# Optimization experiments

Hardware: AMD Instinct MI355X
Metric: run time of the kernel (lower is better)

The kernel has to match this reference:

```python
import jax, jax.numpy as jnp
import numpy as np
import math

N_HEAD = 16
MEM_LEN = 512


def setup_inputs() -> dict:
    key = jax.random.key(0)
    ks = jax.random.split(key, 4)
    B, T, C = 4, 2048, 1024
    x = jax.random.normal(ks[0], (B, T, C), dtype=jnp.float32)
    W_attn = jax.random.normal(ks[1], (C, 3 * C), dtype=jnp.float32) * (1.0 / math.sqrt(C))
    b_attn = jnp.zeros((3 * C,), dtype=jnp.float32)
    W_proj = jax.random.normal(ks[2], (C, C), dtype=jnp.float32) * (1.0 / math.sqrt(C))
    b_proj = jnp.zeros((C,), dtype=jnp.float32)
    return {"x": x, "W_attn": W_attn, "b_attn": b_attn, "W_proj": W_proj, "b_proj": b_proj}


def reference(x, W_attn, b_attn, W_proj, b_proj):
    B, T, C = x.shape
    H = N_HEAD
    Dh = C // H
    # fused qkv projection (torch Linear with weight stored as [in, out])
    qkv = x @ W_attn + b_attn                      # [B, T, 3C]
    q, k, v = jnp.split(qkv, 3, axis=-1)
    q = q.reshape(B, T, H, Dh).transpose(0, 2, 1, 3)  # [B, H, T, Dh]
    k = k.reshape(B, T, H, Dh).transpose(0, 2, 1, 3)
    v = v.reshape(B, T, H, Dh).transpose(0, 2, 1, 3)
    # manual attention: QK^T, causal mask, softmax, att @ V
    att = jnp.einsum('bhtd,bhsd->bhts', q, k) * (1.0 / math.sqrt(Dh))  # [B,H,T,T]
    causal = jnp.tril(jnp.ones((T, T), dtype=bool))
    att = jnp.where(causal[None, None, :, :], att, jnp.finfo(att.dtype).min)
    att = jax.nn.softmax(att, axis=-1)
    y = jnp.einsum('bhts,bhsd->bhtd', att, v)      # [B, H, T, Dh]
    y = y.transpose(0, 2, 1, 3).reshape(B, T, C)
    out = y @ W_proj + b_proj                      # resid_dropout is identity (p=0 / eval)
    new_memory = x[:, -MEM_LEN:, :]
    return out, new_memory
```

## Files before the change

### kernel.cpp

```cpp
#include <hip/hip_runtime.h>
#include <hip/hip_bf16.h>

typedef __bf16 bf16;
typedef __bf16 bf16x8 __attribute__((ext_vector_type(8)));
typedef __bf16 bf16x4v __attribute__((ext_vector_type(4)));
typedef float f32x4 __attribute__((ext_vector_type(4)));
typedef float f32x16 __attribute__((ext_vector_type(16)));
typedef float float4v __attribute__((ext_vector_type(4)));
typedef unsigned int uint32x4 __attribute__((ext_vector_type(4)));

#define MFMA16(a, b, c) __builtin_amdgcn_mfma_f32_16x16x32_bf16(a, b, c, 0, 0, 0)
#define MFMA32(a, b, c) __builtin_amdgcn_mfma_f32_32x32x16_bf16(a, b, c, 0, 0, 0)

#define SCALE_Q 0.1803368801111f

__device__ __forceinline__ void async_load16(const bf16* g, bf16* l) {
    __builtin_amdgcn_global_load_lds(
        (const __attribute__((address_space(1))) void*)g,
        (__attribute__((address_space(3))) void*)l,
        16, 0, 0);
}

__device__ __forceinline__ unsigned int pack2bf(float a, float b) {
    bf16 x = (bf16)a, y = (bf16)b;
    unsigned short ux = __builtin_bit_cast(unsigned short, x);
    unsigned short uy = __builtin_bit_cast(unsigned short, y);
    return (unsigned int)ux | ((unsigned int)uy << 16);
}

__global__ void k_pre(const float* __restrict__ x, const float* __restrict__ W_attn,
                      const float* __restrict__ W_proj,
                      bf16* __restrict__ xb, float* __restrict__ out_mem,
                      bf16* __restrict__ WaT, bf16* __restrict__ WpT) {
    __shared__ float tile[32][33];
    int bid = blockIdx.x;
    if (bid < 8192) {
        int i = bid * 256 + threadIdx.x;
        float4v v = ((const float4v*)x)[i];
        bf16x4v o;
        o.x = (bf16)v.x; o.y = (bf16)v.y; o.z = (bf16)v.z; o.w = (bf16)v.w;
        ((bf16x4v*)xb)[i] = o;
        int rem = i & 524287;
        if (rem >= 393216) {
            int b = i >> 19;
            ((float4v*)out_mem)[(size_t)b * 131072 + (rem - 393216)] = v;
        }
        return;
    }
    const float* W;  bf16* WT;  int R, Cc, bx, by;
    if (bid < 8192 + 3072) {
        int idx = bid - 8192;
        W = W_attn; WT = WaT; R = 1024; Cc = 3072; bx = idx % 96; by = idx / 96;
    } else {
        int idx = bid - 11264;
        W = W_proj; WT = WpT; R = 1024; Cc = 1024; bx = idx & 31; by = idx >> 5;
    }
    int r0 = by * 32, c0 = bx * 32;
    int tx = threadIdx.x & 31, ty = threadIdx.x >> 5;
#pragma unroll
    for (int i = 0; i < 32; i += 8)
        tile[ty + i][tx] = W[(size_t)(r0 + ty + i) * Cc + c0 + tx];
    __syncthreads();
#pragma unroll
    for (int i = 0; i < 32; i += 8)
        WT[(size_t)(c0 + ty + i) * R + r0 + tx] = (bf16)tile[tx][ty + i];
}

#define STAGE64(db, k0) { \
    async_load16(Asrc + (k0),          &As[db][tid8]);         \
    async_load16(Asrc + 32768 + (k0),  &As[db][2048 + tid8]);  \
    async_load16(Asrc + 65536 + (k0),  &As[db][4096 + tid8]);  \
    async_load16(Asrc + 98304 + (k0),  &As[db][6144 + tid8]);  \
    async_load16(Bsrc + (k0),          &Bs[db][tid8]);         \
    async_load16(Bsrc + 32768 + (k0),  &Bs[db][2048 + tid8]);  \
    async_load16(Bsrc + 65536 + (k0),  &Bs[db][4096 + tid8]);  \
    async_load16(Bsrc + 98304 + (k0),  &Bs[db][6144 + tid8]);  }

#define GEMM_BODY64                                                                      \
    STAGE64(0, 0)                                                                        \
    STAGE64(1, 64)                                                                       \
    asm volatile("s_waitcnt vmcnt(8)" ::: "memory");                                     \
    __builtin_amdgcn_sched_barrier(0);                                                   \
    __builtin_amdgcn_s_barrier();                                                        \
    __builtin_amdgcn_sched_barrier(0);                                                   \
    for (int t = 0; t < 16; ++t) {                                                       \
        int db = t & 1;                                                                  \
        _Pragma("unroll")                                                                \
        for (int kc = 0; kc < 2; ++kc) {                                                 \
            bf16x8 af[4], bfr[4];                                                        \
            _Pragma("unroll")                                                            \
            for (int mi = 0; mi < 4; ++mi)                                               \
                af[mi] = *(const bf16x8*)&As[db][(wr * 64 + mi * 16 + lrow) * 64 +       \
                                                 ((kc * 4 + lks) ^ (lrow & 7)) * 8];     \
            _Pragma("unroll")                                                            \
            for (int ni = 0; ni < 4; ++ni)                                               \
                bfr[ni] = *(const bf16x8*)&Bs[db][(wc * 64 + ni * 16 + lrow) * 64 +      \
                                                  ((kc * 4 + lks) ^ (lrow & 7)) * 8];    \
            __builtin_amdgcn_s_setprio(1);                                               \
            _Pragma("unroll")                                                            \
            for (int mi = 0; mi < 4; ++mi)                                               \
                _Pragma("unroll")                                                        \
                for (int ni = 0; ni < 4; ++ni)                                           \
                    acc[mi][ni] = MFMA16(af[mi], bfr[ni], acc[mi][ni]);                  \
            __builtin_amdgcn_s_setprio(0);                                               \
        }                                                                                \
        asm volatile("s_waitcnt lgkmcnt(0)" ::: "memory");                               \
        __builtin_amdgcn_sched_barrier(0);                                               \
        __builtin_amdgcn_s_barrier();                 \
        __builtin_amdgcn_sched_barrier(0);                                               \
        if (t + 2 < 16) {                                                                \
            STAGE64(db, (t + 2) * 64)                \
            asm volatile("s_waitcnt vmcnt(8)" ::: "memory");        \
        } else {                                                                         \
            asm volatile("s_waitcnt vmcnt(0)" ::: "memory");                             \
        }                                                                                \
        __builtin_amdgcn_sched_barrier(0);                                               \
        __builtin_amdgcn_s_barrier();                        \
        __builtin_amdgcn_sched_barrier(0);                                               \
    }

__global__ __launch_bounds__(256, 2) void k_gemm_qkv(
    const bf16* __restrict__ A, const bf16* __restrict__ BT,
    const float* __restrict__ bias,
    bf16* __restrict__ qo, bf16* __restrict__ ko, bf16* __restrict__ vo) {
    __shared__ __align__(16) bf16 As[2][8192];
    __shared__ __align__(16) bf16 Bs[2][8192];
    int orig = blockIdx.y * 24 + blockIdx.x;
    int wg = (orig & 7) * 192 + (orig >> 3);
    int row0 = (wg / 24) * 128;
    int col0 = (wg % 24) * 128;
    int tid = threadIdx.x;
    int lane = tid & 63, w = tid >> 6;
    int wr = w >> 1, wc = w & 1;
    int lrow = lane & 15, lks = lane >> 4;
    int tid8 = tid * 8;
    f32x4 acc[4][4] = {};
    const bf16* Asrc = A + (size_t)(row0 + (tid >> 3)) * 1024 + ((tid & 7) ^ ((tid >> 3) & 7)) * 8;
    const bf16* Bsrc = BT + (size_t)(col0 + (tid >> 3)) * 1024 + ((tid & 7) ^ ((tid >> 3) & 7)) * 8;

    GEMM_BODY64

    int trow = row0 + wr * 64 + lks * 4;
    int tcol = col0 + wc * 64 + lrow;
#pragma unroll
    for (int m = 0; m < 4; ++m)
#pragma unroll
        for (int n = 0; n < 4; ++n) {
            int cg = tcol + n * 16;
            float bi = bias[cg];
#pragma unroll
            for (int j = 0; j < 4; ++j) {
                int rg = trow + m * 16 + j;
                float val = acc[m][n][j] + bi;
                int b = rg >> 11, tt = rg & 2047;
                if (cg < 1024) {
                    int h = cg >> 6, d = cg & 63;
                    size_t base = (size_t)(b * 16 + h) * 131072;
                    size_t idx = base + (size_t)((((tt >> 5) * 4 + (d >> 4)) * 64 + ((d >> 3) & 1) * 32 + (tt & 31)) * 8 + (d & 7));
                    qo[idx] = (bf16)(val * SCALE_Q);
                } else if (cg < 2048) {
                    int c2 = cg - 1024;
                    int h = c2 >> 6, d = c2 & 63;
                    size_t base = (size_t)(b * 16 + h) * 131072;
                    size_t idx = base + (size_t)((((tt >> 5) * 4 + (d >> 4)) * 64 + ((d >> 3) & 1) * 32 + (tt & 31)) * 8 + (d & 7));
                    ko[idx] = (bf16)val;
                } else {
                    int c2 = cg - 2048;
                    int h = c2 >> 6, d = c2 & 63;
                    size_t base = (size_t)(b * 16 + h) * 131072;
                    size_t idx = base + (size_t)(((((tt >> 6) * 4 + ((tt >> 4) & 3)) * 2 + (d >> 5)) * 64 + ((tt >> 3) & 1) * 32 + (d & 31)) * 8 + (tt & 7));
                    vo[idx] = (bf16)val;
                }
            }
        }
}

__global__ __launch_bounds__(256, 2) void k_gemm_proj(
    const bf16* __restrict__ A, const bf16* __restrict__ BT,
    const float* __restrict__ bias, float* __restrict__ out) {
    __shared__ __align__(16) bf16 As[2][8192];
    __shared__ __align__(16) bf16 Bs[2][8192];
    int orig = blockIdx.y * 8 + blockIdx.x;
    int wg = (orig & 7) * 64 + (orig >> 3);
    int row0 = (wg >> 3) * 128;
    int col0 = (wg & 7) * 128;
    int tid = threadIdx.x;
    int lane = tid & 63, w = tid >> 6;
    int wr = w >> 1, wc = w & 1;
    int lrow = lane & 15, lks = lane >> 4;
    int tid8 = tid * 8;
    f32x4 acc[4][4] = {};
    const bf16* Asrc = A + (size_t)(row0 + (tid >> 3)) * 1024 + ((tid & 7) ^ ((tid >> 3) & 7)) * 8;
    const bf16* Bsrc = BT + (size_t)(col0 + (tid >> 3)) * 1024 + ((tid & 7) ^ ((tid >> 3) & 7)) * 8;

    GEMM_BODY64

    int trow = row0 + wr * 64 + lks * 4;
    int tcol = col0 + wc * 64 + lrow;
#pragma unroll
    for (int m = 0; m < 4; ++m)
#pragma unroll
        for (int n = 0; n < 4; ++n) {
            int cg = tcol + n * 16;
            float bi = bias[cg];
#pragma unroll
            for (int j = 0; j < 4; ++j) {
                int rg = trow + m * 16 + j;
                out[(size_t)rg * 1024 + cg] = acc[m][n][j] + bi;
            }
        }
}

__global__ __launch_bounds__(256, 2) void k_attn(
    const bf16* __restrict__ qp, const bf16* __restrict__ kp,
    const bf16* __restrict__ vp, bf16* __restrict__ y) {
    __shared__ __align__(16) bf16 Ks[2][4096];
    __shared__ __align__(16) bf16 Vs[2][4096];
    int id = blockIdx.x;
    int bxp = (id >> 3) & 7;
    int bh = (id & 7) + 8 * (id >> 6);
    int b = bh >> 4;
    int lane = threadIdx.x & 63, w = threadIdx.x >> 6;
    int tl = lane & 31, hi = lane >> 5;
    int lane8 = lane * 8;
    const bf16* Qb = qp + (size_t)bh * 131072;
    const bf16* Kb = kp + (size_t)bh * 131072;
    const bf16* Vb = vp + (size_t)bh * 131072;

    for (int qpass = 0; qpass < 2; ++qpass) {
        int qt0 = (qpass ? 15 - bxp : bxp) * 128;
        int trow0 = qt0 + w * 32;
        int t_g = trow0 + tl;

        bf16x8 qf[4];
        int qs = (trow0 >> 5) * 4;
#pragma unroll
        for (int kc = 0; kc < 4; ++kc)
            qf[kc] = *(const bf16x8*)&Qb[(qs + kc) * 512 + lane8];

        f32x16 o[2] = {};
        float m = -1e30f, l = 0.f;
        int ntb = (qt0 >> 6) + 2;
        int cur = 0;

#pragma unroll
        for (int i = 0; i < 2; ++i) {
            int u = 2 * w + i;
            async_load16(Kb + (size_t)u * 512 + lane8, &Ks[0][u * 512]);
            async_load16(Vb + (size_t)u * 512 + lane8, &Vs[0][u * 512]);
        }
        __syncthreads();

        for (int ti = 0; ti < ntb; ++ti) {
            int s0 = ti * 64;
            if (ti + 1 < ntb) {
#pragma unroll
                for (int i = 0; i < 2; ++i) {
                    int u = 2 * w + i;
                    async_load16(Kb + (size_t)((ti + 1) * 8 + u) * 512 + lane8, &Ks[cur ^ 1][u * 512]);
                    async_load16(Vb + (size_t)((ti + 1) * 8 + u) * 512 + lane8, &Vs[cur ^ 1][u * 512]);
                }
            }
            if (s0 < trow0 + 32) {
                f32x16 accs[2] = {};
                __builtin_amdgcn_s_setprio(1);
#pragma unroll
                for (int st = 0; st < 2; ++st)
#pragma unroll
                    for (int kc = 0; kc < 4; ++kc) {
                        bf16x8 kf = *(const bf16x8*)&Ks[cur][(st * 4 + kc) * 512 + lane8];
                        accs[st] = MFMA32(kf, qf[kc], accs[st]);
                    }
                __builtin_amdgcn_s_setprio(0);

                if (s0 + 63 > trow0) {
#pragma unroll
                    for (int st = 0; st < 2; ++st)
#pragma unroll
                        for (int r = 0; r < 16; ++r) {
                            int s = s0 + st * 32 + (r & 3) + 8 * (r >> 2) + 4 * hi;
                            if (s > t_g) accs[st][r] = -1e30f;
                        }
                }
                float pmax = -1e30f;
#pragma unroll
                for (int st = 0; st < 2; ++st)
#pragma unroll
                    for (int r = 0; r < 16; ++r)
                        pmax = fmaxf(pmax, accs[st][r]);
                pmax = fmaxf(pmax, __shfl_xor(pmax, 32));
                if (!__all(pmax <= m + 8.0f)) {
                    float mn = fmaxf(m, pmax);
                    float corr = __builtin_amdgcn_exp2f(m - mn);
                    m = mn;
                    l *= corr;
#pragma unroll
                    for (int dt = 0; dt < 2; ++dt)
#pragma unroll
                        for (int r = 0; r < 16; ++r)
                            o[dt][r] *= corr;
                }
                float ls = 0.f;
#pragma unroll
                for (int st = 0; st < 2; ++st)
#pragma unroll
                    for (int r = 0; r < 16; ++r) {
                        float p = __builtin_amdgcn_exp2f(accs[st][r] - m);
                        accs[st][r] = p;
                        ls += p;
                    }
                ls += __shfl_xor(ls, 32);
                l += ls;

                unsigned int pk[16];
#pragma unroll
                for (int st = 0; st < 2; ++st)
#pragma unroll
                    for (int q = 0; q < 8; ++q)
                        pk[st * 8 + q] = pack2bf(accs[st][2 * q], accs[st][2 * q + 1]);
                unsigned int rv[8];
#pragma unroll
                for (int st = 0; st < 2; ++st)
#pragma unroll
                    for (int i = 0; i < 4; ++i) {
                        int base = st * 8 + (i < 2 ? i : i + 2);
                        unsigned int send = hi ? pk[base] : pk[base + 2];
                        rv[st * 4 + i] = __shfl_xor(send, 32);
                    }
                __builtin_amdgcn_s_setprio(1);
#pragma unroll
                for (int c = 0; c < 4; ++c) {
                    const int st = c >> 1, c2 = c & 1;
                    uint32x4 pw;
                    pw.x = hi ? rv[st * 4 + 2 * c2]     : pk[st * 8 + 4 * c2];
                    pw.y = hi ? rv[st * 4 + 2 * c2 + 1] : pk[st * 8 + 4 * c2 + 1];
                    pw.z = hi ? pk[st * 8 + 4 * c2 + 2] : rv[st * 4 + 2 * c2];
                    pw.w = hi ? pk[st * 8 + 4 * c2 + 3] : rv[st * 4 + 2 * c2 + 1];
                    bf16x8 pf = __builtin_bit_cast(bf16x8, pw);
#pragma unroll
                    for (int dt = 0; dt < 2; ++dt) {
                        bf16x8 vf = *(const bf16x8*)&Vs[cur][(c * 2 + dt) * 512 + lane8];
                        o[dt] = MFMA32(vf, pf, o[dt]);
                    }
                }
                __builtin_amdgcn_s_setprio(0);
            }
            __syncthreads();
            cur ^= 1;
        }

        int hcol = (bh & 15) * 64;
        float inv = 1.0f / l;
        bf16* yr = y + (size_t)(b * 2048 + t_g) * 1024 + hcol;
#pragma unroll
        for (int dt = 0; dt < 2; ++dt)
#pragma unroll
            for (int rq = 0; rq < 4; ++rq) {
                bf16x4v ov;
#pragma unroll
                for (int ri = 0; ri < 4; ++ri)
                    ov[ri] = (bf16)(o[dt][rq * 4 + ri] * inv);
                *(bf16x4v*)&yr[dt * 32 + rq * 8 + hi * 4] = ov;
            }
    }
}

extern "C" void kernel_launch(void* const* d_in, const int* in_sizes, int n_in,
                              void* d_out, int out_size, void* d_ws, size_t ws_size,
                              hipStream_t stream) {
    const float* x = (const float*)d_in[0];
    const float* W_attn = (const float*)d_in[1];
    const float* b_attn = (const float*)d_in[2];
    const float* W_proj = (const float*)d_in[3];
    const float* b_proj = (const float*)d_in[4];
    float* out = (float*)d_out;
    float* out_mem = out + (size_t)8388608;

    char* ws = (char*)d_ws;
    bf16* xb  = (bf16*)(ws);
    bf16* WaT = (bf16*)(ws + ((size_t)16 << 20));
    bf16* WpT = (bf16*)(ws + ((size_t)22 << 20));
    bf16* q   = (bf16*)(ws + ((size_t)24 << 20));
    bf16* k   = (bf16*)(ws + ((size_t)40 << 20));
    bf16* vT  = (bf16*)(ws + ((size_t)56 << 20));
    bf16* y   = (bf16*)(ws + ((size_t)72 << 20));

    k_pre<<<12288, 256, 0, stream>>>(x, W_attn, W_proj, xb, out_mem, WaT, WpT);
    k_gemm_qkv<<<dim3(24, 64), 256, 0, stream>>>(xb, WaT, b_attn, q, k, vT);
    k_attn<<<512, 256, 0, stream>>>(q, k, vT, y);
    k_gemm_proj<<<dim3(8, 64), 256, 0, stream>>>(y, WpT, b_proj, out);
}
```

Before: 184.1 us.

## Pre-pack GEMM operands in MFMA fragment order and load directly into registers

The preprocessing kernel and the attention epilogue now write x, both weight matrices and the attention output in a packed layout where each 16-row, 32-k fragment is contiguous in per-lane order. The two GEMMs then drop LDS staging and barriers and load fragments straight from global memory into registers, double-buffered in registers. This removes LDS traffic and synchronization, but it gives up LDS-based reuse across waves, so each wave reads its A and B fragments from global memory or L2 separately. The weight packing kernel also reads W with a stride instead of coalesced rows.

Measured after the change: 179.9 us. 2.3% less time.

```diff
diff --git a/kernel.cpp b/kernel.cpp
--- a/kernel.cpp
+++ b/kernel.cpp
@@ -28,117 +28,110 @@
     return (unsigned int)ux | ((unsigned int)uy << 16);
 }
 
+
 __global__ void k_pre(const float* __restrict__ x, const float* __restrict__ W_attn,
                       const float* __restrict__ W_proj,
-                      bf16* __restrict__ xb, float* __restrict__ out_mem,
-                      bf16* __restrict__ WaT, bf16* __restrict__ WpT) {
-    __shared__ float tile[32][33];
-    int bid = blockIdx.x;
-    if (bid < 8192) {
-        int i = bid * 256 + threadIdx.x;
-        float4v v = ((const float4v*)x)[i];
-        bf16x4v o;
-        o.x = (bf16)v.x; o.y = (bf16)v.y; o.z = (bf16)v.z; o.w = (bf16)v.w;
-        ((bf16x4v*)xb)[i] = o;
-        int rem = i & 524287;
-        if (rem >= 393216) {
-            int b = i >> 19;
-            ((float4v*)out_mem)[(size_t)b * 131072 + (rem - 393216)] = v;
-        }
-        return;
+                      bf16* __restrict__ xpk, float* __restrict__ out_mem,
+                      bf16* __restrict__ Wapk, bf16* __restrict__ Wppk) {
+    int bid = blockIdx.x, tid = threadIdx.x;
+    int lane = tid & 63;
+    if (bid < 4096) {
+        int line = bid * 4 + (tid >> 6);
+        int slab = line >> 5, kc = line & 31;
+        int t = slab * 16 + (lane & 15);
+        int k = kc * 32 + (lane >> 4) * 8;
+        const float* src = x + (size_t)t * 1024 + k;
+        float4v v0 = *(const float4v*)src;
+        float4v v1 = *(const float4v*)(src + 4);
+        bf16x8 o;
+        o[0] = (bf16)v0.x; o[1] = (bf16)v0.y; o[2] = (bf16)v0.z; o[3] = (bf16)v0.w;
+        o[4] = (bf16)v1.x; o[5] = (bf16)v1.y; o[6] = (bf16)v1.z; o[7] = (bf16)v1.w;
+        *(bf16x8*)(xpk + (size_t)line * 512 + lane * 8) = o;
+        int tb = t & 2047;
+        if (tb >= 1536) {
+            float* dst = out_mem + ((size_t)(t >> 11) * 512 + (tb - 1536)) * 1024 + k;
+            *(float4v*)dst = v0;
+            *(float4v*)(dst + 4) = v1;
+        }
+    } else if (bid < 4096 + 1536) {
+        int line = (bid - 4096) * 4 + (tid >> 6);
+        int slab = line >> 5, kc = line & 31;
+        int n = slab * 16 + (lane & 15);
+        int k = kc * 32 + (lane >> 4) * 8;
+        bf16x8 o;
+#pragma unroll
+        for (int j = 0; j < 8; ++j)
+            o[j] = (bf16)W_attn[(size_t)(k + j) * 3072 + n];
+        *(bf16x8*)(Wapk + (size_t)line * 512 + lane * 8) = o;
+    } else {
+        int line = (bid - 5632) * 4 + (tid >> 6);
+        int slab = line >> 5, kc = line & 31;
+        int n = slab * 16 + (lane & 15);
+        int k = kc * 32 + (lane >> 4) * 8;
+        bf16x8 o;
+#pragma unroll
+        for (int j = 0; j < 8; ++j)
+            o[j] = (bf16)W_proj[(size_t)(k + j) * 1024 + n];
+        *(bf16x8*)(Wppk + (size_t)line * 512 + lane * 8) = o;
     }
-    const float* W;  bf16* WT;  int R, Cc, bx, by;
-    if (bid < 8192 + 3072) {
-        int idx = bid - 8192;
-        W = W_attn; WT = WaT; R = 1024; Cc = 3072; bx = idx % 96; by = idx / 96;
-    } else {
-        int idx = bid - 11264;
-        W = W_proj; WT = WpT; R = 1024; Cc = 1024; bx = idx & 31; by = idx >> 5;
+}
+
+#define GEMM_NOLDS_BODY                                                                  \
+    const bf16* Ab[4]; const bf16* Bb[4];                                                \
+    _Pragma("unroll")                                                                    \
+    for (int m = 0; m < 4; ++m)                                                          \
+        Ab[m] = Apk + (size_t)(((row0 >> 4) + wr * 4 + m) * 32) * 512 + lane * 8;        \
+    _Pragma("unroll")                                                                    \
+    for (int n = 0; n < 4; ++n)                                                          \
+        Bb[n] = Bpk + (size_t)(((col0 >> 4) + wc * 4 + n) * 32) * 512 + lane * 8;        \
+    f32x4 acc[4][4] = {};                                                                \
+    bf16x8 a0[4], b0[4], a1[4], b1[4];                                                   \
+    _Pragma("unroll")                                                                    \
+    for (int m = 0; m < 4; ++m) a0[m] = *(const bf16x8*)(Ab[m]);                         \
+    _Pragma("unroll")                                                                    \
+    for (int n = 0; n < 4; ++n) b0[n] = *(const bf16x8*)(Bb[n]);                         \
+    for (int t = 0; t < 16; ++t) {                                                       \
+        int o1 = (2 * t + 1) * 512;                                                      \
+        _Pragma("unroll")                                                                \
+        for (int m = 0; m < 4; ++m) a1[m] = *(const bf16x8*)(Ab[m] + o1);                \
+        _Pragma("unroll")                                                                \
+        for (int n = 0; n < 4; ++n) b1[n] = *(const bf16x8*)(Bb[n] + o1);                \
+        __builtin_amdgcn_s_setprio(1);                                                   \
+        _Pragma("unroll")                                                                \
+        for (int m = 0; m < 4; ++m)                                                      \
+            _Pragma("unroll")                                                            \
+            for (int n = 0; n < 4; ++n)                                                  \
+                acc[m][n] = MFMA16(a0[m], b0[n], acc[m][n]);                             \
+        __builtin_amdgcn_s_setprio(0);                                                   \
+        if (t < 15) {                                                                    \
+            int o2 = (2 * t + 2) * 512;                                                  \
+            _Pragma("unroll")                                                            \
+            for (int m = 0; m < 4; ++m) a0[m] = *(const bf16x8*)(Ab[m] + o2);            \
+            _Pragma("unroll")                                                            \
+            for (int n = 0; n < 4; ++n) b0[n] = *(const bf16x8*)(Bb[n] + o2);            \
+        }                                                                                \
+        __builtin_amdgcn_s_setprio(1);                                                   \
+        _Pragma("unroll")                                                                \
+        for (int m = 0; m < 4; ++m)                                                      \
+            _Pragma("unroll")                                                            \
+            for (int n = 0; n < 4; ++n)                                                  \
+                acc[m][n] = MFMA16(a1[m], b1[n], acc[m][n]);                             \
+        __builtin_amdgcn_s_setprio(0);                                                   \
     }
-    int r0 = by * 32, c0 = bx * 32;
-    int tx = threadIdx.x & 31, ty = threadIdx.x >> 5;
-#pragma unroll
-    for (int i = 0; i < 32; i += 8)
-        tile[ty + i][tx] = W[(size_t)(r0 + ty + i) * Cc + c0 + tx];
-    __syncthreads();
-#pragma unroll
-    for (int i = 0; i < 32; i += 8)
-        WT[(size_t)(c0 + ty + i) * R + r0 + tx] = (bf16)tile[tx][ty + i];
-}
-
-#define STAGE64(db, k0) { \
-    async_load16(Asrc + (k0),          &As[db][tid8]);         \
-    async_load16(Asrc + 32768 + (k0),  &As[db][2048 + tid8]);  \
-    async_load16(Asrc + 65536 + (k0),  &As[db][4096 + tid8]);  \
-    async_load16(Asrc + 98304 + (k0),  &As[db][6144 + tid8]);  \
-    async_load16(Bsrc + (k0),          &Bs[db][tid8]);         \
-    async_load16(Bsrc + 32768 + (k0),  &Bs[db][2048 + tid8]);  \
-    async_load16(Bsrc + 65536 + (k0),  &Bs[db][4096 + tid8]);  \
-    async_load16(Bsrc + 98304 + (k0),  &Bs[db][6144 + tid8]);  }
-
-#define GEMM_BODY64                                                                      \
-    STAGE64(0, 0)                                                                        \
-    STAGE64(1, 64)                                                                       \
-    asm volatile("s_waitcnt vmcnt(8)" ::: "memory");                                     \
-    __builtin_amdgcn_sched_barrier(0);                                                   \
-    __builtin_amdgcn_s_barrier();                                                        \
-    __builtin_amdgcn_sched_barrier(0);                                                   \
-    for (int t = 0; t < 16; ++t) {                                                       \
-        int db = t & 1;                                                                  \
-        _Pragma("unroll")                                                                \
-        for (int kc = 0; kc < 2; ++kc) {                                                 \
-            bf16x8 af[4], bfr[4];                                                        \
-            _Pragma("unroll")                                                            \
-            for (int mi = 0; mi < 4; ++mi)                                               \
-                af[mi] = *(const bf16x8*)&As[db][(wr * 64 + mi * 16 + lrow) * 64 +       \
-                                                 ((kc * 4 + lks) ^ (lrow & 7)) * 8];     \
-            _Pragma("unroll")                                                            \
-            for (int ni = 0; ni < 4; ++ni)                                               \
-                bfr[ni] = *(const bf16x8*)&Bs[db][(wc * 64 + ni * 16 + lrow) * 64 +      \
-                                                  ((kc * 4 + lks) ^ (lrow & 7)) * 8];    \
-            __builtin_amdgcn_s_setprio(1);                                               \
-            _Pragma("unroll")                                                            \
-            for (int mi = 0; mi < 4; ++mi)                                               \
-                _Pragma("unroll")                                                        \
-                for (int ni = 0; ni < 4; ++ni)                                           \
-                    acc[mi][ni] = MFMA16(af[mi], bfr[ni], acc[mi][ni]);                  \
-            __builtin_amdgcn_s_setprio(0);                                               \
-        }                                                                                \
-        asm volatile("s_waitcnt lgkmcnt(0)" ::: "memory");                               \
-        __builtin_amdgcn_sched_barrier(0);                                               \
-        __builtin_amdgcn_s_barrier();                 \
-        __builtin_amdgcn_sched_barrier(0);                                               \
-        if (t + 2 < 16) {                                                                \
-            STAGE64(db, (t + 2) * 64)                \
-            asm volatile("s_waitcnt vmcnt(8)" ::: "memory");        \
-        } else {                                                                         \
-            asm volatile("s_waitcnt vmcnt(0)" ::: "memory");                             \
-        }                                                                                \
-        __builtin_amdgcn_sched_barrier(0);                                               \
-        __builtin_amdgcn_s_barrier();                        \
-        __builtin_amdgcn_sched_barrier(0);                                               \
-    }
 
 __global__ __launch_bounds__(256, 2) void k_gemm_qkv(
-    const bf16* __restrict__ A, const bf16* __restrict__ BT,
+    const bf16* __restrict__ Apk, const bf16* __restrict__ Bpk,
     const float* __restrict__ bias,
     bf16* __restrict__ qo, bf16* __restrict__ ko, bf16* __restrict__ vo) {
-    __shared__ __align__(16) bf16 As[2][8192];
-    __shared__ __align__(16) bf16 Bs[2][8192];
-    int orig = blockIdx.y * 24 + blockIdx.x;
+    int orig = blockIdx.x;
     int wg = (orig & 7) * 192 + (orig >> 3);
     int row0 = (wg / 24) * 128;
     int col0 = (wg % 24) * 128;
-    int tid = threadIdx.x;
-    int lane = tid & 63, w = tid >> 6;
+    int lane = threadIdx.x & 63, w = threadIdx.x >> 6;
     int wr = w >> 1, wc = w & 1;
     int lrow = lane & 15, lks = lane >> 4;
-    int tid8 = tid * 8;
-    f32x4 acc[4][4] = {};
-    const bf16* Asrc = A + (size_t)(row0 + (tid >> 3)) * 1024 + ((tid & 7) ^ ((tid >> 3) & 7)) * 8;
-    const bf16* Bsrc = BT + (size_t)(col0 + (tid >> 3)) * 1024 + ((tid & 7) ^ ((tid >> 3) & 7)) * 8;
-
-    GEMM_BODY64
+
+    GEMM_NOLDS_BODY
 
     int trow = row0 + wr * 64 + lks * 4;
     int tcol = col0 + wc * 64 + lrow;
@@ -176,24 +169,17 @@
 }
 
 __global__ __launch_bounds__(256, 2) void k_gemm_proj(
-    const bf16* __restrict__ A, const bf16* __restrict__ BT,
+    const bf16* __restrict__ Apk, const bf16* __restrict__ Bpk,
     const float* __restrict__ bias, float* __restrict__ out) {
-    __shared__ __align__(16) bf16 As[2][8192];
-    __shared__ __align__(16) bf16 Bs[2][8192];
-    int orig = blockIdx.y * 8 + blockIdx.x;
+    int orig = blockIdx.x;
     int wg = (orig & 7) * 64 + (orig >> 3);
     int row0 = (wg >> 3) * 128;
     int col0 = (wg & 7) * 128;
-    int tid = threadIdx.x;
-    int lane = tid & 63, w = tid >> 6;
+    int lane = threadIdx.x & 63, w = threadIdx.x >> 6;
     int wr = w >> 1, wc = w & 1;
     int lrow = lane & 15, lks = lane >> 4;
-    int tid8 = tid * 8;
-    f32x4 acc[4][4] = {};
-    const bf16* Asrc = A + (size_t)(row0 + (tid >> 3)) * 1024 + ((tid & 7) ^ ((tid >> 3) & 7)) * 8;
-    const bf16* Bsrc = BT + (size_t)(col0 + (tid >> 3)) * 1024 + ((tid & 7) ^ ((tid >> 3) & 7)) * 8;
-
-    GEMM_BODY64
+
+    GEMM_NOLDS_BODY
 
     int trow = row0 + wr * 64 + lks * 4;
     int tcol = col0 + wc * 64 + lrow;
@@ -213,7 +199,7 @@
 
 __global__ __launch_bounds__(256, 2) void k_attn(
     const bf16* __restrict__ qp, const bf16* __restrict__ kp,
-    const bf16* __restrict__ vp, bf16* __restrict__ y) {
+    const bf16* __restrict__ vp, bf16* __restrict__ ypk) {
     __shared__ __align__(16) bf16 Ks[2][4096];
     __shared__ __align__(16) bf16 Vs[2][4096];
     int id = blockIdx.x;
@@ -349,9 +335,10 @@
             cur ^= 1;
         }
 
-        int hcol = (bh & 15) * 64;
+        int grow = b * 2048 + t_g;
+        int slab = grow >> 4;
+        int hkc = (bh & 15) * 2;
         float inv = 1.0f / l;
-        bf16* yr = y + (size_t)(b * 2048 + t_g) * 1024 + hcol;
 #pragma unroll
         for (int dt = 0; dt < 2; ++dt)
 #pragma unroll
@@ -360,7 +347,8 @@
 #pragma unroll
                 for (int ri = 0; ri < 4; ++ri)
                     ov[ri] = (bf16)(o[dt][rq * 4 + ri] * inv);
-                *(bf16x4v*)&yr[dt * 32 + rq * 8 + hi * 4] = ov;
+                size_t idx = (size_t)(slab * 32 + hkc + dt) * 512 + rq * 128 + (grow & 15) * 8 + 4 * hi;
+                *(bf16x4v*)&ypk[idx] = ov;
             }
     }
 }
@@ -377,16 +365,16 @@
     float* out_mem = out + (size_t)8388608;
 
     char* ws = (char*)d_ws;
-    bf16* xb  = (bf16*)(ws);
-    bf16* WaT = (bf16*)(ws + ((size_t)16 << 20));
-    bf16* WpT = (bf16*)(ws + ((size_t)22 << 20));
-    bf16* q   = (bf16*)(ws + ((size_t)24 << 20));
-    bf16* k   = (bf16*)(ws + ((size_t)40 << 20));
-    bf16* vT  = (bf16*)(ws + ((size_t)56 << 20));
-    bf16* y   = (bf16*)(ws + ((size_t)72 << 20));
-
-    k_pre<<<12288, 256, 0, stream>>>(x, W_attn, W_proj, xb, out_mem, WaT, WpT);
-    k_gemm_qkv<<<dim3(24, 64), 256, 0, stream>>>(xb, WaT, b_attn, q, k, vT);
-    k_attn<<<512, 256, 0, stream>>>(q, k, vT, y);
-    k_gemm_proj<<<dim3(8, 64), 256, 0, stream>>>(y, WpT, b_proj, out);
-}
+    bf16* xpk  = (bf16*)(ws);
+    bf16* Wapk = (bf16*)(ws + ((size_t)16 << 20));
+    bf16* Wppk = (bf16*)(ws + ((size_t)22 << 20));
+    bf16* q    = (bf16*)(ws + ((size_t)24 << 20));
+    bf16* k    = (bf16*)(ws + ((size_t)40 << 20));
+    bf16* vT   = (bf16*)(ws + ((size_t)56 << 20));
+    bf16* ypk  = (bf16*)(ws + ((size_t)72 << 20));
+
+    k_pre<<<6144, 256, 0, stream>>>(x, W_attn, W_proj, xpk, out_mem, Wapk, Wppk);
+    k_gemm_qkv<<<1536, 256, 0, stream>>>(xpk, Wapk, b_attn, q, k, vT);
+    k_attn<<<512, 256, 0, stream>>>(q, k, vT, ypk);
+    k_gemm_proj<<<512, 256, 0, stream>>>(ypk, Wppk, b_proj, out);
+}
```
